# Performance work log

Measured on AMD Instinct MI355X. Metric: run time of the kernel, lower is better.

Reference implementation:

```python
import jax, jax.numpy as jnp
import numpy as np

B, S, E, H = 2, 2048, 1024, 16
D = E // H
SCALE = D ** -0.5


def setup_inputs() -> dict:
    key = jax.random.key(0)
    k1, k2, k3, k4, k5 = jax.random.split(key, 5)
    x = jax.random.normal(k1, (B, S, E), dtype=jnp.float32)
    # torch Linear weights: [out, in]
    W_attn = jax.random.normal(k2, (3 * E, E), dtype=jnp.float32) * (E ** -0.5)
    b_attn = jax.random.normal(k3, (3 * E,), dtype=jnp.float32) * 0.02
    W_proj = jax.random.normal(k4, (E, E), dtype=jnp.float32) * (E ** -0.5)
    b_proj = jax.random.normal(k5, (E,), dtype=jnp.float32) * 0.02
    mask = jnp.tril(jnp.ones((S, S), dtype=jnp.int32))[None, None]  # causal [1,1,S,S]
    return {"x": x, "W_attn": W_attn, "b_attn": b_attn,
            "W_proj": W_proj, "b_proj": b_proj, "mask": mask}


def reference(x, W_attn, b_attn, W_proj, b_proj, mask):
    # fused qkv projection: [B,S,3E]
    qkv = jnp.einsum('bse,fe->bsf', x, W_attn) + b_attn
    q, k, v = jnp.split(qkv, 3, axis=-1)
    # split heads -> [B,H,S,D]
    def heads(t):
        return t.reshape(B, S, H, D).transpose(0, 2, 1, 3)
    q, k, v = heads(q), heads(k), heads(v)
    # scaled dot-product attention with causal mask
    w = jnp.einsum('bhqd,bhkd->bhqk', q, k) * SCALE
    w = jnp.where(mask == 0, jnp.finfo(w.dtype).min, w)
    w = jax.nn.softmax(w, axis=-1)  # attn dropout p=0 (eval)
    o = jnp.einsum('bhqk,bhkd->bhqd', w, v)
    # merge heads -> [B,S,E]
    o = o.transpose(0, 2, 1, 3).reshape(B, S, E)
    out = jnp.einsum('bse,fe->bsf', o, W_proj) + b_proj  # resid dropout p=0
    return out
```

## Files before the change

kernel.cpp:

```cpp
#include <hip/hip_runtime.h>
#include <hip/hip_bf16.h>

typedef unsigned short u16;
typedef unsigned int u32;
typedef float f32x4 __attribute__((ext_vector_type(4)));
typedef short bf16x8 __attribute__((ext_vector_type(8)));

#define BB 2
#define SS 2048
#define EE 1024
#define HH 16
#define DD 64
#define QSCALE 0.18033688011f

__device__ __forceinline__ u16 f2bf(float f) {
    union { u32 i; float f; } x; x.f = f;
    return (u16)((x.i + 0x7FFFu + ((x.i >> 16) & 1u)) >> 16);
}
__device__ __forceinline__ u32 pkbf(float a, float b) {
    __hip_bfloat162 h = __float22bfloat162_rn(make_float2(a, b));
    union { __hip_bfloat162 h; u32 u; } c; c.h = h; return c.u;
}

#define MFMA16(a, b, c) __builtin_amdgcn_mfma_f32_16x16x32_bf16((a), (b), (c), 0, 0, 0)

__device__ __forceinline__ void gld16(const u16* g, u16* l) {
    __builtin_amdgcn_global_load_lds(
        (const __attribute__((address_space(1))) void*)g,
        (__attribute__((address_space(3))) void*)l,
        16, 0, 0);
}

__global__ __launch_bounds__(256) void convert_all(
    const float* __restrict__ x, const float* __restrict__ wa,
    const float* __restrict__ wp, u16* __restrict__ dst)
{
    const size_t n0 = (size_t)4096 * 1024;
    const size_t n1 = n0 + (size_t)3072 * 1024;
    size_t i = ((size_t)blockIdx.x * 256 + threadIdx.x) * 4;
    const float* s;
    size_t off;
    if (i < n0)      { s = x;  off = 0;  }
    else if (i < n1) { s = wa; off = n0; }
    else             { s = wp; off = n1; }
    float4 v = *(const float4*)(s + (i - off));
    uint2 o;
    o.x = pkbf(v.x, v.y);
    o.y = pkbf(v.z, v.w);
    *(uint2*)(dst + i) = o;
}

__global__ __launch_bounds__(512, 4) void gemm_qkv(
    const u16* __restrict__ A, const u16* __restrict__ B, const float* __restrict__ bias,
    u16* __restrict__ Qo, u16* __restrict__ Ko, u16* __restrict__ Vto)
{
    __shared__ __align__(16) u16 SMEM[16384];
    u16* As = SMEM;
    u16* Bs = SMEM + 8192;
    const int n0 = blockIdx.x * 128, m0 = blockIdx.y * 128;
    const int tid = threadIdx.x;
    const int wave = tid >> 6, lane = tid & 63;
    const int l16 = lane & 15, quad = lane >> 4;
    const int wm = wave >> 2, wn = wave & 3;
    const int ldr = lane >> 3;
    const int csw = ((lane & 7) ^ ldr) * 8;

    f32x4 acc[4][2];
#pragma unroll
    for (int i = 0; i < 4; ++i)
#pragma unroll
        for (int j = 0; j < 2; ++j) acc[i][j] = f32x4{0.f, 0.f, 0.f, 0.f};

    const int aorb = wave >> 2;
    u16* stgbuf = aorb ? Bs : As;
    const u16* stgsrc = aorb ? B : A;
    const int stgbase = aorb ? n0 : m0;

    for (int k0 = 0; k0 < 1024; k0 += 64) {
        __syncthreads();
#pragma unroll
        for (int t = 0; t < 4; ++t) {
            const int c = (wave & 3) * 4 + t;
            const int row = c * 8 + ldr;
            gld16(stgsrc + (size_t)(stgbase + row) * 1024 + k0 + csw,
                  &stgbuf[c * 512 + lane * 8]);
        }
        __syncthreads();
#pragma unroll
        for (int ks = 0; ks < 2; ++ks) {
            bf16x8 af[4], bf[2];
#pragma unroll
            for (int i = 0; i < 4; ++i)
                af[i] = *(const bf16x8*)&As[(wm * 64 + i * 16 + l16) * 64 +
                                            ((ks * 4 + quad) ^ (l16 & 7)) * 8];
#pragma unroll
            for (int j = 0; j < 2; ++j)
                bf[j] = *(const bf16x8*)&Bs[(wn * 32 + j * 16 + l16) * 64 +
                                            ((ks * 4 + quad) ^ (l16 & 7)) * 8];
#pragma unroll
            for (int i = 0; i < 4; ++i)
#pragma unroll
                for (int j = 0; j < 2; ++j)
                    acc[i][j] = MFMA16(af[i], bf[j], acc[i][j]);
        }
    }

    const int part = blockIdx.x >> 3;
    const int hbase = (blockIdx.x & 7) << 1;
    if (part != 2) {
        const int h = hbase + (wn >> 1);
#pragma unroll
        for (int j = 0; j < 2; ++j) {
            const int f = n0 + wn * 32 + j * 16 + l16;
            const int d = f & 63;
            const float bj = bias[f];
#pragma unroll
            for (int i = 0; i < 4; ++i) {
#pragma unroll
                for (int r = 0; r < 4; ++r) {
                    const int m = m0 + wm * 64 + i * 16 + quad * 4 + r;
                    const int b = m >> 11, s = m & 2047;
                    const float val = acc[i][j][r] + bj;
                    if (part == 0)
                        Qo[(((size_t)(b * HH + h)) * SS + s) * DD + d] = f2bf(val * QSCALE);
                    else
                        Ko[(((size_t)(b * HH + h)) * SS + s) * DD + d] = f2bf(val);
                }
            }
        }
    } else {
        u16* T = SMEM;
#pragma unroll
        for (int wmr = 0; wmr < 2; ++wmr) {
            __syncthreads();
            if (wm == wmr) {
#pragma unroll
                for (int j = 0; j < 2; ++j) {
                    const float bj = bias[n0 + wn * 32 + j * 16 + l16];
#pragma unroll
                    for (int i = 0; i < 4; ++i) {
                        uint2 pw;
                        pw.x = pkbf(acc[i][j][0] + bj, acc[i][j][1] + bj);
                        pw.y = pkbf(acc[i][j][2] + bj, acc[i][j][3] + bj);
                        *(uint2*)&T[(wn * 32 + j * 16 + l16) * 72 + i * 16 + quad * 4] = pw;
                    }
                }
            }
            __syncthreads();
            const int frow = tid >> 2;
            const int qtr = tid & 3;
            const int h = hbase + (frow >> 6);
            const int d = frow & 63;
            const int mg = m0 + wmr * 64;
            const int b = mg >> 11, sbase = mg & 2047;
            u16* dstrow = Vto + (((size_t)(b * HH + h)) * DD + d) * SS + sbase;
#pragma unroll
            for (int l = 0; l < 4; ++l) {
                const int mo = qtr * 16 + l * 4;
                *(uint2*)(dstrow + mo) = *(const uint2*)&T[frow * 72 + mo];
            }
        }
    }
}

__global__ __launch_bounds__(512, 4) void gemm_proj(
    const u16* __restrict__ A, const u16* __restrict__ B, const float* __restrict__ bias,
    float* __restrict__ out)
{
    __shared__ __align__(16) u16 SMEM[12288];
    u16* As = SMEM;
    u16* Bs = SMEM + 4096;
    const int n0 = blockIdx.x * 128, m0 = blockIdx.y * 64;
    const int tid = threadIdx.x;
    const int wave = tid >> 6, lane = tid & 63;
    const int l16 = lane & 15, quad = lane >> 4;
    const int wm = wave >> 2, wn = wave & 3;
    const int ldr = lane >> 3;
    const int csw = ((lane & 7) ^ ldr) * 8;

    f32x4 acc[2][2];
#pragma unroll
    for (int i = 0; i < 2; ++i)
#pragma unroll
        for (int j = 0; j < 2; ++j) acc[i][j] = f32x4{0.f, 0.f, 0.f, 0.f};

    for (int k0 = 0; k0 < 1024; k0 += 64) {
        __syncthreads();
#pragma unroll
        for (int t = 0; t < 3; ++t) {
            const int c = wave * 3 + t;
            if (c < 8) {
                const int row = c * 8 + ldr;
                gld16(A + (size_t)(m0 + row) * 1024 + k0 + csw, &As[c * 512 + lane * 8]);
            } else {
                const int c2 = c - 8;
                const int row = c2 * 8 + ldr;
                gld16(B + (size_t)(n0 + row) * 1024 + k0 + csw, &Bs[c2 * 512 + lane * 8]);
            }
        }
        __syncthreads();
#pragma unroll
        for (int ks = 0; ks < 2; ++ks) {
            bf16x8 af[2], bf[2];
#pragma unroll
            for (int i = 0; i < 2; ++i)
                af[i] = *(const bf16x8*)&As[(wm * 32 + i * 16 + l16) * 64 +
                                            ((ks * 4 + quad) ^ (l16 & 7)) * 8];
#pragma unroll
            for (int j = 0; j < 2; ++j)
                bf[j] = *(const bf16x8*)&Bs[(wn * 32 + j * 16 + l16) * 64 +
                                            ((ks * 4 + quad) ^ (l16 & 7)) * 8];
#pragma unroll
            for (int i = 0; i < 2; ++i)
#pragma unroll
                for (int j = 0; j < 2; ++j)
                    acc[i][j] = MFMA16(af[i], bf[j], acc[i][j]);
        }
    }
#pragma unroll
    for (int j = 0; j < 2; ++j) {
        const int f = n0 + wn * 32 + j * 16 + l16;
        const float bj = bias[f];
#pragma unroll
        for (int i = 0; i < 2; ++i) {
#pragma unroll
            for (int r = 0; r < 4; ++r) {
                const int m = m0 + wm * 32 + i * 16 + quad * 4 + r;
                out[(size_t)m * EE + f] = acc[i][j][r] + bj;
            }
        }
    }
}

__global__ __launch_bounds__(256, 2) void attn(
    const u16* __restrict__ Q, const u16* __restrict__ K, const u16* __restrict__ VT,
    u16* __restrict__ O)
{
    const int p = blockIdx.y;
    const int bh = blockIdx.x;
    const int tid = threadIdx.x;
    const int wave = tid >> 6, lane = tid & 63;
    const int l16 = lane & 15, quad = lane >> 4;
    const int ldr = lane >> 3;
    const int csw = ((lane & 7) ^ ldr) * 8;
    __shared__ __align__(16) u16 Ks[2][2][64 * 64];
    __shared__ __align__(16) u16 Vts[2][2][64 * 64];
    __shared__ __align__(16) u16 Ps[64 * 72];

    const u16* qptr = Q + (size_t)bh * SS * DD;
    const u16* kptr = K + (size_t)bh * SS * DD;
    const u16* vtptr = VT + (size_t)bh * DD * SS;
    const int b = bh >> 4, h = bh & 15;

    auto stage = [&](int t, int buf, int sub) {
#pragma unroll
        for (int c = 0; c < 2; ++c) {
            const int a0 = wave * 2 + c;
            const int row = a0 * 8 + ldr;
            gld16(kptr + (size_t)(t * 64 + row) * DD + csw,
                  &Ks[buf][sub][a0 * 512 + lane * 8]);
            gld16(vtptr + (size_t)row * SS + t * 64 + csw,
                  &Vts[buf][sub][a0 * 512 + lane * 8]);
        }
    };

    for (int half = 0; half < 2; ++half) {
        const int qb = half ? p : 31 - p;
        const int qrow = qb * 64 + wave * 16 + l16;
        bf16x8 bq[2];
#pragma unroll
        for (int ks = 0; ks < 2; ++ks)
            bq[ks] = *(const bf16x8*)(qptr + (size_t)qrow * DD + ks * 32 + quad * 8);

        float lp = 0.f;
        f32x4 o_acc[4];
#pragma unroll
        for (int j = 0; j < 4; ++j) o_acc[j] = f32x4{0.f, 0.f, 0.f, 0.f};

        auto tile_compute = [&](const u16* Kb, const u16* Vb, int t) {
            f32x4 s[4];
#pragma unroll
            for (int j = 0; j < 4; ++j) s[j] = f32x4{0.f, 0.f, 0.f, 0.f};
            __builtin_amdgcn_s_setprio(1);
#pragma unroll
            for (int ks = 0; ks < 2; ++ks) {
#pragma unroll
                for (int j = 0; j < 4; ++j) {
                    bf16x8 ak = *(const bf16x8*)&Kb[(j * 16 + l16) * 64 +
                                                    ((ks * 4 + quad) ^ (l16 & 7)) * 8];
                    s[j] = MFMA16(ak, bq[ks], s[j]);
                }
            }
            __builtin_amdgcn_s_setprio(0);
            if (t == qb) {
#pragma unroll
                for (int j = 0; j < 4; ++j)
#pragma unroll
                    for (int r = 0; r < 4; ++r) {
                        const int key = t * 64 + j * 16 + quad * 4 + r;
                        if (key > qrow) s[j][r] = -INFINITY;
                    }
            }
#pragma unroll
            for (int j = 0; j < 4; ++j) {
                const float p0 = __builtin_amdgcn_exp2f(s[j][0]);
                const float p1 = __builtin_amdgcn_exp2f(s[j][1]);
                const float p2 = __builtin_amdgcn_exp2f(s[j][2]);
                const float p3 = __builtin_amdgcn_exp2f(s[j][3]);
                lp += (p0 + p1) + (p2 + p3);
                uint2 pw; pw.x = pkbf(p0, p1); pw.y = pkbf(p2, p3);
                *(uint2*)&Ps[(wave * 16 + l16) * 72 + j * 16 + quad * 4] = pw;
            }
            __builtin_amdgcn_s_setprio(1);
#pragma unroll
            for (int ks = 0; ks < 2; ++ks) {
                bf16x8 bp = *(const bf16x8*)&Ps[(wave * 16 + l16) * 72 + ks * 32 + quad * 8];
#pragma unroll
                for (int j = 0; j < 4; ++j) {
                    bf16x8 av = *(const bf16x8*)&Vb[(j * 16 + l16) * 64 +
                                                    ((ks * 4 + quad) ^ (l16 & 7)) * 8];
                    o_acc[j] = MFMA16(av, bp, o_acc[j]);
                }
            }
            __builtin_amdgcn_s_setprio(0);
        };

        __syncthreads();
        stage(0, 0, 0);
        stage(qb < 1 ? qb : 1, 0, 1);

        for (int kb = 0; kb <= qb; kb += 2) {
            const int cur = (kb >> 1) & 1;
            __syncthreads();
            if (kb + 2 <= qb) {
                stage(kb + 2, cur ^ 1, 0);
                const int t3 = kb + 3 > qb ? qb : kb + 3;
                stage(t3, cur ^ 1, 1);
            }
            tile_compute(Ks[cur][0], Vts[cur][0], kb);
            if (kb + 1 <= qb)
                tile_compute(Ks[cur][1], Vts[cur][1], kb + 1);
        }

        float l = lp;
        l += __shfl_xor(l, 16);
        l += __shfl_xor(l, 32);
        const float inv = 1.0f / l;
#pragma unroll
        for (int j = 0; j < 4; ++j) {
            uint2 o4;
            o4.x = pkbf(o_acc[j][0] * inv, o_acc[j][1] * inv);
            o4.y = pkbf(o_acc[j][2] * inv, o_acc[j][3] * inv);
            *(uint2*)&O[((size_t)(b * SS + qrow)) * EE + h * DD + j * 16 + quad * 4] = o4;
        }
    }
}

extern "C" void kernel_launch(void* const* d_in, const int* in_sizes, int n_in,
                              void* d_out, int out_size, void* d_ws, size_t ws_size,
                              hipStream_t stream) {
    const float* x      = (const float*)d_in[0];
    const float* W_attn = (const float*)d_in[1];
    const float* b_attn = (const float*)d_in[2];
    const float* W_proj = (const float*)d_in[3];
    const float* b_proj = (const float*)d_in[4];
    float* out = (float*)d_out;

    u16* xb  = (u16*)d_ws;
    u16* wab = xb + (size_t)4096 * 1024;
    u16* wpb = wab + (size_t)3072 * 1024;
    u16* qw  = wpb + (size_t)1024 * 1024;
    u16* kw  = qw + (size_t)BB * HH * SS * DD;
    u16* vtw = kw + (size_t)BB * HH * SS * DD;
    u16* ow  = xb;

    convert_all<<<8192, 256, 0, stream>>>(x, W_attn, W_proj, xb);
    gemm_qkv<<<dim3(24, 32), 512, 0, stream>>>(xb, wab, b_attn, qw, kw, vtw);
    attn<<<dim3(32, 16), 256, 0, stream>>>(qw, kw, vtw, ow);
    gemm_proj<<<dim3(8, 64), 512, 0, stream>>>(ow, wpb, b_proj, out);
}
```

Before: 181.1 us.

## Double-buffer LDS tiles in QKV and projection GEMMs

Both GEMM kernels now keep two shared-memory tile buffers. Each loop iteration starts the global-to-LDS load for the next K tile before running the MFMAs on the current one, which leaves a single barrier per iteration. The aim is to hide global load latency behind matrix math. In exchange, each block uses twice as much LDS, which may cut how many blocks fit on a CU. The attention kernel is unchanged.

Measured after the change: 180.2 us. No clear change (-0.5%).

```diff
diff --git a/kernel.cpp b/kernel.cpp
--- a/kernel.cpp
+++ b/kernel.cpp
@@ -54,9 +54,7 @@
     const u16* __restrict__ A, const u16* __restrict__ B, const float* __restrict__ bias,
     u16* __restrict__ Qo, u16* __restrict__ Ko, u16* __restrict__ Vto)
 {
-    __shared__ __align__(16) u16 SMEM[16384];
-    u16* As = SMEM;
-    u16* Bs = SMEM + 8192;
+    __shared__ __align__(16) u16 SMEM[2][16384];
     const int n0 = blockIdx.x * 128, m0 = blockIdx.y * 128;
     const int tid = threadIdx.x;
     const int wave = tid >> 6, lane = tid & 63;
@@ -72,12 +70,12 @@
         for (int j = 0; j < 2; ++j) acc[i][j] = f32x4{0.f, 0.f, 0.f, 0.f};
 
     const int aorb = wave >> 2;
-    u16* stgbuf = aorb ? Bs : As;
     const u16* stgsrc = aorb ? B : A;
     const int stgbase = aorb ? n0 : m0;
-
-    for (int k0 = 0; k0 < 1024; k0 += 64) {
-        __syncthreads();
+    const int stgoff = aorb ? 8192 : 0;
+
+    auto stage = [&](int k0, int buf) {
+        u16* stgbuf = &SMEM[buf][stgoff];
 #pragma unroll
         for (int t = 0; t < 4; ++t) {
             const int c = (wave & 3) * 4 + t;
@@ -85,7 +83,15 @@
             gld16(stgsrc + (size_t)(stgbase + row) * 1024 + k0 + csw,
                   &stgbuf[c * 512 + lane * 8]);
         }
+    };
+
+    stage(0, 0);
+    for (int k0 = 0; k0 < 1024; k0 += 64) {
+        const int cur = (k0 >> 6) & 1;
         __syncthreads();
+        if (k0 + 64 < 1024) stage(k0 + 64, cur ^ 1);
+        const u16* As = SMEM[cur];
+        const u16* Bs = SMEM[cur] + 8192;
 #pragma unroll
         for (int ks = 0; ks < 2; ++ks) {
             bf16x8 af[4], bf[2];
@@ -129,7 +135,7 @@
             }
         }
     } else {
-        u16* T = SMEM;
+        u16* T = SMEM[0];
 #pragma unroll
         for (int wmr = 0; wmr < 2; ++wmr) {
             __syncthreads();
@@ -167,9 +173,7 @@
     const u16* __restrict__ A, const u16* __restrict__ B, const float* __restrict__ bias,
     float* __restrict__ out)
 {
-    __shared__ __align__(16) u16 SMEM[12288];
-    u16* As = SMEM;
-    u16* Bs = SMEM + 4096;
+    __shared__ __align__(16) u16 SMEM[2][12288];
     const int n0 = blockIdx.x * 128, m0 = blockIdx.y * 64;
     const int tid = threadIdx.x;
     const int wave = tid >> 6, lane = tid & 63;
@@ -184,21 +188,30 @@
 #pragma unroll
         for (int j = 0; j < 2; ++j) acc[i][j] = f32x4{0.f, 0.f, 0.f, 0.f};
 
-    for (int k0 = 0; k0 < 1024; k0 += 64) {
-        __syncthreads();
+    auto stage = [&](int k0, int buf) {
 #pragma unroll
         for (int t = 0; t < 3; ++t) {
             const int c = wave * 3 + t;
             if (c < 8) {
                 const int row = c * 8 + ldr;
-                gld16(A + (size_t)(m0 + row) * 1024 + k0 + csw, &As[c * 512 + lane * 8]);
+                gld16(A + (size_t)(m0 + row) * 1024 + k0 + csw,
+                      &SMEM[buf][c * 512 + lane * 8]);
             } else {
                 const int c2 = c - 8;
                 const int row = c2 * 8 + ldr;
-                gld16(B + (size_t)(n0 + row) * 1024 + k0 + csw, &Bs[c2 * 512 + lane * 8]);
-            }
-        }
+                gld16(B + (size_t)(n0 + row) * 1024 + k0 + csw,
+                      &SMEM[buf][4096 + c2 * 512 + lane * 8]);
+            }
+        }
+    };
+
+    stage(0, 0);
+    for (int k0 = 0; k0 < 1024; k0 += 64) {
+        const int cur = (k0 >> 6) & 1;
         __syncthreads();
+        if (k0 + 64 < 1024) stage(k0 + 64, cur ^ 1);
+        const u16* As = SMEM[cur];
+        const u16* Bs = SMEM[cur] + 4096;
 #pragma unroll
         for (int ks = 0; ks < 2; ++ks) {
             bf16x8 af[2], bf[2];
```
